# Performance work log

Hardware: AMD Instinct MI355X
Metric: run time of the kernel (lower is better)

Reference implementation:

```python
import jax, jax.numpy as jnp
import numpy as np

KT = 1.0

def l2norm(x, eps=1e-12):
    # torch F.normalize(p=2): x / max(||x||, eps)
    n = jnp.sqrt(jnp.sum(x * x, axis=-1, keepdims=True))
    return x / jnp.maximum(n, eps)

def setup_inputs() -> dict:
    key = jax.random.key(0)
    k1, k2, k3 = jax.random.split(key, 3)
    B, T, key_dim, e_dim, n_e = 16, 1024, 256, 256, 512
    key_soft = jax.random.normal(k1, (B, T, key_dim), dtype=jnp.float32)
    # embedding tables init uniform(-1/n_e, 1/n_e) as in the torch module
    keys = jax.random.uniform(k2, (n_e, key_dim), minval=-1.0 / n_e, maxval=1.0 / n_e, dtype=jnp.float32)
    vparams = jax.random.uniform(k3, (n_e, e_dim), minval=-1.0 / n_e, maxval=1.0 / n_e, dtype=jnp.float32)
    return {"key_soft": key_soft, "keys": keys, "vparams": vparams}

def reference(key_soft, keys, vparams):
    # clustering_forward of VQClassifierNN
    ksn = l2norm(key_soft)                                  # [B,T,D]
    keys_norm = l2norm(keys)                                # [n_e,D]
    score_ksh = jnp.einsum('btd,nd->btn', ksn, keys_norm)   # [B,T,n_e]
    score_kss = jnp.einsum('btd,bsd->bts', ksn, ksn)        # [B,T,T]
    # softmax weighting over codebook (score_to_weight)
    w = jax.nn.softmax(score_ksh / KT, axis=-1)
    w = jnp.nan_to_num(w)
    vp_norm = l2norm(vparams)                               # [n_e,E]
    vparams_w = l2norm(jnp.einsum('btn,ne->bte', w, vp_norm))  # [B,T,E]
    score_vpss = jnp.einsum('bte,bse->bts', vparams_w, vparams_w)  # [B,T,T]
    score_vpsh = jnp.einsum('bte,ne->btn', vparams_w, vp_norm)     # [B,T,n_e]
    encoding_indices = jnp.argmax(score_ksh, axis=-1)       # [B,T] int
    vparams_hard = l2norm(vparams[encoding_indices])        # gather + normalize
    # straight-through: grads flow through vparams_w
    vparams_hard = vparams_w + jax.lax.stop_gradient(vparams_hard - vparams_w)
    return (encoding_indices, vparams_w, vparams_hard,
            score_vpss, score_vpsh, score_kss, score_ksh)
```

## Files before the change

kernel.cpp:

```cpp
#include <hip/hip_runtime.h>
#include <hip/hip_bf16.h>

#define BB 16
#define TT 1024
#define DD 256
#define NE 512
#define BT 16384

typedef unsigned short ushort_t;
typedef __attribute__((ext_vector_type(8))) short bf16x8;
typedef __attribute__((ext_vector_type(4))) float f32x4;

#define AS_GLOBAL __attribute__((address_space(1)))
#define AS_SHARED __attribute__((address_space(3)))

static __device__ __forceinline__ ushort_t f2bf(float f) {
    union { float f; unsigned u; } x; x.f = f;
    unsigned r = x.u + 0x7fffu + ((x.u >> 16) & 1u);
    return (ushort_t)(r >> 16);
}

__global__ __launch_bounds__(256) void l2norm_dual(const float* __restrict__ in,
                                                   float* __restrict__ out,
                                                   ushort_t* __restrict__ out_bf) {
    const int row = blockIdx.x;
    const long long base = (long long)row * DD;
    const int t = threadIdx.x;
    float v = in[base + t];
    float ss = v * v;
    #pragma unroll
    for (int off = 32; off > 0; off >>= 1) ss += __shfl_down(ss, off, 64);
    __shared__ float partial[4];
    const int wave = t >> 6, lane = t & 63;
    if (lane == 0) partial[wave] = ss;
    __syncthreads();
    __shared__ float s_inv;
    if (t == 0) {
        float tot = partial[0] + partial[1] + partial[2] + partial[3];
        s_inv = 1.0f / fmaxf(sqrtf(tot), 1e-12f);
    }
    __syncthreads();
    const float r = v * s_inv;
    out[base + t] = r;
    if (out_bf) out_bf[base + t] = f2bf(r);
}

__global__ void transpose_bf(const float* __restrict__ in, ushort_t* __restrict__ out,
                             int rows, int cols) {
    int idx = blockIdx.x * blockDim.x + threadIdx.x;
    if (idx < rows * cols) {
        int r = idx / cols, c = idx - r * cols;
        out[(long long)c * rows + r] = f2bf(in[idx]);
    }
}

__global__ __launch_bounds__(256) void gemm_nt(const float* __restrict__ A,
                                               const float* __restrict__ Bm,
                                               float* __restrict__ C,
                                               int M, int N, int K) {
    const int bm = blockIdx.y * 128;
    const int bn = blockIdx.x * 128;

    __shared__ float As[16][132];
    __shared__ float Bs[16][132];

    const int tid = threadIdx.x;
    const int tx = tid & 15;
    const int ty = tid >> 4;
    const int r  = tid >> 2;
    const int c4 = tid & 3;

    float acc[8][8] = {};

    for (int k0 = 0; k0 < K; k0 += 16) {
        #pragma unroll
        for (int i = 0; i < 2; ++i) {
            const int rr = r + i * 64;
            float4 va = *(const float4*)(A + (long long)(bm + rr) * K + k0 + c4 * 4);
            As[c4 * 4 + 0][rr] = va.x;
            As[c4 * 4 + 1][rr] = va.y;
            As[c4 * 4 + 2][rr] = va.z;
            As[c4 * 4 + 3][rr] = va.w;
            float4 vb = *(const float4*)(Bm + (long long)(bn + rr) * K + k0 + c4 * 4);
            Bs[c4 * 4 + 0][rr] = vb.x;
            Bs[c4 * 4 + 1][rr] = vb.y;
            Bs[c4 * 4 + 2][rr] = vb.z;
            Bs[c4 * 4 + 3][rr] = vb.w;
        }
        __syncthreads();
        #pragma unroll
        for (int k = 0; k < 16; ++k) {
            float a[8], b[8];
            *(float4*)&a[0] = *(const float4*)&As[k][ty * 8];
            *(float4*)&a[4] = *(const float4*)&As[k][ty * 8 + 4];
            *(float4*)&b[0] = *(const float4*)&Bs[k][tx * 8];
            *(float4*)&b[4] = *(const float4*)&Bs[k][tx * 8 + 4];
            #pragma unroll
            for (int i = 0; i < 8; ++i)
                #pragma unroll
                for (int j = 0; j < 8; ++j)
                    acc[i][j] = fmaf(a[i], b[j], acc[i][j]);
        }
        __syncthreads();
    }

    #pragma unroll
    for (int i = 0; i < 8; ++i) {
        float* dst = C + (long long)(bm + ty * 8 + i) * N + bn + tx * 8;
        *(float4*)dst       = make_float4(acc[i][0], acc[i][1], acc[i][2], acc[i][3]);
        *(float4*)(dst + 4) = make_float4(acc[i][4], acc[i][5], acc[i][6], acc[i][7]);
    }
}

__global__ __launch_bounds__(256) void gemm_bf16_nt(const ushort_t* __restrict__ A,
                                                    const ushort_t* __restrict__ Bm,
                                                    float* __restrict__ C,
                                                    int M, int N, int K,
                                                    long long sA, long long sB, long long sC) {
    A  += sA * blockIdx.z;
    Bm += sB * blockIdx.z;
    C  += sC * blockIdx.z;
    const int bm = blockIdx.y * 128;
    const int bn = blockIdx.x * 128;

    __shared__ ushort_t As[128 * 32];
    __shared__ ushort_t Bs[128 * 32];

    const int tid = threadIdx.x;
    const int wv = tid >> 6;
    const int ln = tid & 63;

    const int srow   = ln >> 2;
    const int schunk = (ln & 3) * 8;

    const int wm = (wv >> 1) * 64;
    const int wn = (wv & 1) * 64;
    const int fr = ln & 15;
    const int fq = (ln >> 4) * 8;

    f32x4 acc[4][4] = {};

    for (int k0 = 0; k0 < K; k0 += 32) {
        #pragma unroll
        for (int t = 0; t < 2; ++t) {
            const int ra = wv * 32 + t * 16;
            const ushort_t* ga = A + (long long)(bm + ra + srow) * K + k0 + schunk;
            __builtin_amdgcn_global_load_lds((const AS_GLOBAL void*)ga,
                                             (AS_SHARED void*)&As[ra * 32], 16, 0, 0);
            const ushort_t* gb = Bm + (long long)(bn + ra + srow) * K + k0 + schunk;
            __builtin_amdgcn_global_load_lds((const AS_GLOBAL void*)gb,
                                             (AS_SHARED void*)&Bs[ra * 32], 16, 0, 0);
        }
        __syncthreads();

        bf16x8 af[4], bfr[4];
        #pragma unroll
        for (int i = 0; i < 4; ++i)
            af[i] = *(const bf16x8*)&As[(wm + i * 16 + fr) * 32 + fq];
        #pragma unroll
        for (int j = 0; j < 4; ++j)
            bfr[j] = *(const bf16x8*)&Bs[(wn + j * 16 + fr) * 32 + fq];
        #pragma unroll
        for (int i = 0; i < 4; ++i)
            #pragma unroll
            for (int j = 0; j < 4; ++j)
                acc[i][j] = __builtin_amdgcn_mfma_f32_16x16x32_bf16(af[i], bfr[j], acc[i][j], 0, 0, 0);
        __syncthreads();
    }

    const int col  = ln & 15;
    const int qrow = (ln >> 4) * 4;
    #pragma unroll
    for (int i = 0; i < 4; ++i)
        #pragma unroll
        for (int j = 0; j < 4; ++j) {
            #pragma unroll
            for (int r = 0; r < 4; ++r)
                C[(long long)(bm + wm + i * 16 + qrow + r) * N + bn + wn + j * 16 + col] = acc[i][j][r];
        }
}

__global__ __launch_bounds__(256) void softmax_argmax(const float* __restrict__ S,
                                                      float* __restrict__ idx_out,
                                                      ushort_t* __restrict__ W) {
    const int row = blockIdx.x;
    const long long base = (long long)row * NE;
    const int t = threadIdx.x;
    const float v0 = S[base + t];
    const float v1 = S[base + t + 256];

    float bv; int bi;
    if (v1 > v0) { bv = v1; bi = t + 256; } else { bv = v0; bi = t; }
    #pragma unroll
    for (int off = 32; off > 0; off >>= 1) {
        float ov = __shfl_down(bv, off, 64);
        int   oi = __shfl_down(bi, off, 64);
        if (ov > bv || (ov == bv && oi < bi)) { bv = ov; bi = oi; }
    }
    __shared__ float pv[4];
    __shared__ int   pi[4];
    const int wave = t >> 6, lane = t & 63;
    if (lane == 0) { pv[wave] = bv; pi[wave] = bi; }
    __syncthreads();
    __shared__ float s_max;
    __shared__ int   s_idx;
    if (t == 0) {
        bv = pv[0]; bi = pi[0];
        #pragma unroll
        for (int k = 1; k < 4; ++k)
            if (pv[k] > bv || (pv[k] == bv && pi[k] < bi)) { bv = pv[k]; bi = pi[k]; }
        s_max = bv; s_idx = bi;
    }
    __syncthreads();
    const float m = s_max;
    const float e0 = expf(v0 - m);
    const float e1 = expf(v1 - m);
    float ssum = e0 + e1;
    #pragma unroll
    for (int off = 32; off > 0; off >>= 1) ssum += __shfl_down(ssum, off, 64);
    __shared__ float ps[4];
    if (lane == 0) ps[wave] = ssum;
    __syncthreads();
    __shared__ float s_sum;
    if (t == 0) s_sum = ps[0] + ps[1] + ps[2] + ps[3];
    __syncthreads();
    const float inv = 1.0f / s_sum;
    W[base + t]       = f2bf(e0 * inv);
    W[base + t + 256] = f2bf(e1 * inv);
    if (t == 0) idx_out[row] = (float)s_idx;
}

__global__ __launch_bounds__(256) void vpw_finish(const float* __restrict__ raw,
                                                  const float* __restrict__ idxf,
                                                  const float* __restrict__ vp_norm,
                                                  float* __restrict__ vpw,
                                                  ushort_t* __restrict__ vpw_bf,
                                                  float* __restrict__ vph) {
    const int row = blockIdx.x;
    const long long base = (long long)row * DD;
    const int t = threadIdx.x;
    const float v = raw[base + t];
    float ss = v * v;
    #pragma unroll
    for (int off = 32; off > 0; off >>= 1) ss += __shfl_down(ss, off, 64);
    __shared__ float partial[4];
    const int wave = t >> 6, lane = t & 63;
    if (lane == 0) partial[wave] = ss;
    __syncthreads();
    __shared__ float s_inv;
    if (t == 0) {
        float tot = partial[0] + partial[1] + partial[2] + partial[3];
        s_inv = 1.0f / fmaxf(sqrtf(tot), 1e-12f);
    }
    __syncthreads();
    const float r = v * s_inv;
    vpw[base + t] = r;
    vpw_bf[base + t] = f2bf(r);
    const int idx = (int)idxf[row];
    vph[base + t] = vp_norm[(long long)idx * DD + t];
}

extern "C" void kernel_launch(void* const* d_in, const int* in_sizes, int n_in,
                              void* d_out, int out_size, void* d_ws, size_t ws_size,
                              hipStream_t stream) {
    const float* key_soft = (const float*)d_in[0];
    const float* keys     = (const float*)d_in[1];
    const float* vparams  = (const float*)d_in[2];
    float* out = (float*)d_out;

    const long long off0 = 0;
    const long long off1 = off0 + BT;
    const long long off2 = off1 + (long long)BT * DD;
    const long long off3 = off2 + (long long)BT * DD;
    const long long off4 = off3 + (long long)BB * TT * TT;
    const long long off5 = off4 + (long long)BT * NE;
    const long long off6 = off5 + (long long)BB * TT * TT;

    float* o_idx  = out + off0;
    float* o_vpw  = out + off1;
    float* o_vph  = out + off2;
    float* o_vpss = out + off3;
    float* o_vpsh = out + off4;
    float* o_kss  = out + off5;
    float* o_ksh  = out + off6;

    float*    keys_n  = (float*)d_ws;
    float*    vp_n    = keys_n + (long long)NE * DD;
    ushort_t* vp_n_bf = (ushort_t*)(vp_n + (long long)NE * DD);
    ushort_t* vpnT_bf = vp_n_bf + (long long)NE * DD;
    ushort_t* vpw_bf  = vpnT_bf + (long long)DD * NE;

    float*    ksn     = o_kss;
    ushort_t* ksn_bf  = (ushort_t*)o_vpsh;
    float*    raw_scr = o_vpss;
    ushort_t* w_bf    = (ushort_t*)(o_vpss + (long long)BT * DD);

    l2norm_dual<<<BT, 256, 0, stream>>>(key_soft, ksn, ksn_bf);
    l2norm_dual<<<NE, 256, 0, stream>>>(keys, keys_n, (ushort_t*)nullptr);
    l2norm_dual<<<NE, 256, 0, stream>>>(vparams, vp_n, vp_n_bf);
    transpose_bf<<<(NE * DD + 255) / 256, 256, 0, stream>>>(vp_n, vpnT_bf, NE, DD);

    gemm_nt<<<dim3(NE / 128, BT / 128, 1), 256, 0, stream>>>(
        ksn, keys_n, o_ksh, BT, NE, DD);

    softmax_argmax<<<BT, 256, 0, stream>>>(o_ksh, o_idx, w_bf);

    gemm_bf16_nt<<<dim3(DD / 128, BT / 128, 1), 256, 0, stream>>>(
        w_bf, vpnT_bf, raw_scr, BT, DD, NE, 0, 0, 0);

    gemm_bf16_nt<<<dim3(TT / 128, TT / 128, BB), 256, 0, stream>>>(
        ksn_bf, ksn_bf, o_kss, TT, TT, DD,
        (long long)TT * DD, (long long)TT * DD, (long long)TT * TT);

    vpw_finish<<<BT, 256, 0, stream>>>(raw_scr, o_idx, vp_n, o_vpw, vpw_bf, o_vph);

    gemm_bf16_nt<<<dim3(TT / 128, TT / 128, BB), 256, 0, stream>>>(
        vpw_bf, vpw_bf, o_vpss, TT, TT, DD,
        (long long)TT * DD, (long long)TT * DD, (long long)TT * TT);

    gemm_bf16_nt<<<dim3(NE / 128, BT / 128, 1), 256, 0, stream>>>(
        vpw_bf, vp_n_bf, o_vpsh, BT, NE, DD, 0, 0, 0);
}
```

Baseline: 387.4 us.

## Compute ksh scores with bf16 MFMA and rescore argmax candidates in fp32

Replaces the fp32 SIMT GEMM for the key/codebook scores with the bf16 MFMA GEMM. To keep argmax exact, the softmax kernel collects codes within 0.01 of the max and recomputes their dot products in fp32 before choosing the index. The codebook transpose is folded into the l2norm kernel, which removes one launch. The stored score_ksh output and the softmax weights now carry bf16 rounding error, and more than 128 near-max candidates would be truncated.

New measurement: 388.4 us. Within noise of the previous version (+0.3%).

```diff
diff --git a/kernel.cpp b/kernel.cpp
--- a/kernel.cpp
+++ b/kernel.cpp
@@ -22,7 +22,9 @@
 
 __global__ __launch_bounds__(256) void l2norm_dual(const float* __restrict__ in,
                                                    float* __restrict__ out,
-                                                   ushort_t* __restrict__ out_bf) {
+                                                   ushort_t* __restrict__ out_bf,
+                                                   ushort_t* __restrict__ out_bf_T,
+                                                   int rows) {
     const int row = blockIdx.x;
     const long long base = (long long)row * DD;
     const int t = threadIdx.x;
@@ -43,73 +45,7 @@
     const float r = v * s_inv;
     out[base + t] = r;
     if (out_bf) out_bf[base + t] = f2bf(r);
-}
-
-__global__ void transpose_bf(const float* __restrict__ in, ushort_t* __restrict__ out,
-                             int rows, int cols) {
-    int idx = blockIdx.x * blockDim.x + threadIdx.x;
-    if (idx < rows * cols) {
-        int r = idx / cols, c = idx - r * cols;
-        out[(long long)c * rows + r] = f2bf(in[idx]);
-    }
-}
-
-__global__ __launch_bounds__(256) void gemm_nt(const float* __restrict__ A,
-                                               const float* __restrict__ Bm,
-                                               float* __restrict__ C,
-                                               int M, int N, int K) {
-    const int bm = blockIdx.y * 128;
-    const int bn = blockIdx.x * 128;
-
-    __shared__ float As[16][132];
-    __shared__ float Bs[16][132];
-
-    const int tid = threadIdx.x;
-    const int tx = tid & 15;
-    const int ty = tid >> 4;
-    const int r  = tid >> 2;
-    const int c4 = tid & 3;
-
-    float acc[8][8] = {};
-
-    for (int k0 = 0; k0 < K; k0 += 16) {
-        #pragma unroll
-        for (int i = 0; i < 2; ++i) {
-            const int rr = r + i * 64;
-            float4 va = *(const float4*)(A + (long long)(bm + rr) * K + k0 + c4 * 4);
-            As[c4 * 4 + 0][rr] = va.x;
-            As[c4 * 4 + 1][rr] = va.y;
-            As[c4 * 4 + 2][rr] = va.z;
-            As[c4 * 4 + 3][rr] = va.w;
-            float4 vb = *(const float4*)(Bm + (long long)(bn + rr) * K + k0 + c4 * 4);
-            Bs[c4 * 4 + 0][rr] = vb.x;
-            Bs[c4 * 4 + 1][rr] = vb.y;
-            Bs[c4 * 4 + 2][rr] = vb.z;
-            Bs[c4 * 4 + 3][rr] = vb.w;
-        }
-        __syncthreads();
-        #pragma unroll
-        for (int k = 0; k < 16; ++k) {
-            float a[8], b[8];
-            *(float4*)&a[0] = *(const float4*)&As[k][ty * 8];
-            *(float4*)&a[4] = *(const float4*)&As[k][ty * 8 + 4];
-            *(float4*)&b[0] = *(const float4*)&Bs[k][tx * 8];
-            *(float4*)&b[4] = *(const float4*)&Bs[k][tx * 8 + 4];
-            #pragma unroll
-            for (int i = 0; i < 8; ++i)
-                #pragma unroll
-                for (int j = 0; j < 8; ++j)
-                    acc[i][j] = fmaf(a[i], b[j], acc[i][j]);
-        }
-        __syncthreads();
-    }
-
-    #pragma unroll
-    for (int i = 0; i < 8; ++i) {
-        float* dst = C + (long long)(bm + ty * 8 + i) * N + bn + tx * 8;
-        *(float4*)dst       = make_float4(acc[i][0], acc[i][1], acc[i][2], acc[i][3]);
-        *(float4*)(dst + 4) = make_float4(acc[i][4], acc[i][5], acc[i][6], acc[i][7]);
-    }
+    if (out_bf_T) out_bf_T[(long long)t * rows + row] = f2bf(r);
 }
 
 __global__ __launch_bounds__(256) void gemm_bf16_nt(const ushort_t* __restrict__ A,
@@ -180,39 +116,71 @@
         }
 }
 
-__global__ __launch_bounds__(256) void softmax_argmax(const float* __restrict__ S,
-                                                      float* __restrict__ idx_out,
-                                                      ushort_t* __restrict__ W) {
+#define RS_CAP 128
+__global__ __launch_bounds__(256) void softmax_argmax_rescore(
+        const float* __restrict__ S,
+        const float* __restrict__ ksn,
+        const float* __restrict__ keys_n,
+        float* __restrict__ idx_out,
+        ushort_t* __restrict__ W) {
     const int row = blockIdx.x;
     const long long base = (long long)row * NE;
     const int t = threadIdx.x;
     const float v0 = S[base + t];
     const float v1 = S[base + t + 256];
 
-    float bv; int bi;
-    if (v1 > v0) { bv = v1; bi = t + 256; } else { bv = v0; bi = t; }
-    #pragma unroll
-    for (int off = 32; off > 0; off >>= 1) {
-        float ov = __shfl_down(bv, off, 64);
-        int   oi = __shfl_down(bi, off, 64);
-        if (ov > bv || (ov == bv && oi < bi)) { bv = ov; bi = oi; }
-    }
+    __shared__ float q[DD];
+    q[t] = ksn[(long long)row * DD + t];
+
+    float bv = fmaxf(v0, v1);
+    #pragma unroll
+    for (int off = 32; off > 0; off >>= 1) bv = fmaxf(bv, __shfl_down(bv, off, 64));
     __shared__ float pv[4];
-    __shared__ int   pi[4];
     const int wave = t >> 6, lane = t & 63;
-    if (lane == 0) { pv[wave] = bv; pi[wave] = bi; }
+    if (lane == 0) pv[wave] = bv;
     __syncthreads();
     __shared__ float s_max;
-    __shared__ int   s_idx;
-    if (t == 0) {
-        bv = pv[0]; bi = pi[0];
-        #pragma unroll
-        for (int k = 1; k < 4; ++k)
-            if (pv[k] > bv || (pv[k] == bv && pi[k] < bi)) { bv = pv[k]; bi = pi[k]; }
-        s_max = bv; s_idx = bi;
+    __shared__ int   s_cnt;
+    if (t == 0) {
+        s_max = fmaxf(fmaxf(pv[0], pv[1]), fmaxf(pv[2], pv[3]));
+        s_cnt = 0;
     }
     __syncthreads();
     const float m = s_max;
+
+    __shared__ int   cidx[RS_CAP];
+    __shared__ float cval[RS_CAP];
+    const float EPS = 0.01f;
+    if (v0 >= m - EPS) {
+        int slot = atomicAdd(&s_cnt, 1);
+        if (slot < RS_CAP) cidx[slot] = t;
+    }
+    if (v1 >= m - EPS) {
+        int slot = atomicAdd(&s_cnt, 1);
+        if (slot < RS_CAP) cidx[slot] = t + 256;
+    }
+    __syncthreads();
+    const int ncand = min(s_cnt, RS_CAP);
+
+    if (t < ncand) {
+        const float* kr = keys_n + (long long)cidx[t] * DD;
+        float s = 0.0f;
+        #pragma unroll 8
+        for (int i = 0; i < DD; ++i) s = fmaf(q[i], kr[i], s);
+        cval[t] = s;
+    }
+    __syncthreads();
+    __shared__ int s_idx;
+    if (t == 0) {
+        float best = cval[0]; int bi = cidx[0];
+        for (int j = 1; j < ncand; ++j) {
+            if (cval[j] > best || (cval[j] == best && cidx[j] < bi)) {
+                best = cval[j]; bi = cidx[j];
+            }
+        }
+        s_idx = bi;
+    }
+
     const float e0 = expf(v0 - m);
     const float e1 = expf(v1 - m);
     float ssum = e0 + e1;
@@ -284,26 +252,26 @@
     float* o_kss  = out + off5;
     float* o_ksh  = out + off6;
 
-    float*    keys_n  = (float*)d_ws;
-    float*    vp_n    = keys_n + (long long)NE * DD;
-    ushort_t* vp_n_bf = (ushort_t*)(vp_n + (long long)NE * DD);
-    ushort_t* vpnT_bf = vp_n_bf + (long long)NE * DD;
-    ushort_t* vpw_bf  = vpnT_bf + (long long)DD * NE;
+    float*    keys_n    = (float*)d_ws;
+    float*    vp_n      = keys_n + (long long)NE * DD;
+    ushort_t* keys_n_bf = (ushort_t*)(vp_n + (long long)NE * DD);
+    ushort_t* vp_n_bf   = keys_n_bf + (long long)NE * DD;
+    ushort_t* vpnT_bf   = vp_n_bf + (long long)NE * DD;
+    ushort_t* vpw_bf    = vpnT_bf + (long long)DD * NE;
 
     float*    ksn     = o_kss;
     ushort_t* ksn_bf  = (ushort_t*)o_vpsh;
     float*    raw_scr = o_vpss;
     ushort_t* w_bf    = (ushort_t*)(o_vpss + (long long)BT * DD);
 
-    l2norm_dual<<<BT, 256, 0, stream>>>(key_soft, ksn, ksn_bf);
-    l2norm_dual<<<NE, 256, 0, stream>>>(keys, keys_n, (ushort_t*)nullptr);
-    l2norm_dual<<<NE, 256, 0, stream>>>(vparams, vp_n, vp_n_bf);
-    transpose_bf<<<(NE * DD + 255) / 256, 256, 0, stream>>>(vp_n, vpnT_bf, NE, DD);
-
-    gemm_nt<<<dim3(NE / 128, BT / 128, 1), 256, 0, stream>>>(
-        ksn, keys_n, o_ksh, BT, NE, DD);
-
-    softmax_argmax<<<BT, 256, 0, stream>>>(o_ksh, o_idx, w_bf);
+    l2norm_dual<<<BT, 256, 0, stream>>>(key_soft, ksn, ksn_bf, (ushort_t*)nullptr, BT);
+    l2norm_dual<<<NE, 256, 0, stream>>>(keys, keys_n, keys_n_bf, (ushort_t*)nullptr, NE);
+    l2norm_dual<<<NE, 256, 0, stream>>>(vparams, vp_n, vp_n_bf, vpnT_bf, NE);
+
+    gemm_bf16_nt<<<dim3(NE / 128, BT / 128, 1), 256, 0, stream>>>(
+        ksn_bf, keys_n_bf, o_ksh, BT, NE, DD, 0, 0, 0);
+
+    softmax_argmax_rescore<<<BT, 256, 0, stream>>>(o_ksh, ksn, keys_n, o_idx, w_bf);
 
     gemm_bf16_nt<<<dim3(DD / 128, BT / 128, 1), 256, 0, stream>>>(
         w_bf, vpnT_bf, raw_scr, BT, DD, NE, 0, 0, 0);
```
